# Kernel tuning notes

Hardware: AMD Instinct MI355X
Metric: run time of the kernel (lower is better)

Reference implementation:

```python
import jax, jax.numpy as jnp
import numpy as np

# ---- static config (seq_lens / is_prefill are Python lists in the original) ----
HIDDEN, H, D = 4096, 32, 128
SEQ = 1024            # prefill length / decode history length
N_PRE, N_DEC = 4, 4
T = N_PRE * SEQ + N_DEC            # 4100 total tokens
SEQ_LENS = [SEQ] * N_PRE + [SEQ] * N_DEC
IS_PREFILL = [True] * N_PRE + [False] * N_DEC
NUM_SLOTS = 8192
MAX_LEN, ROPE_BASE = 8192, 10000.0
SCALE = D ** -0.5


def _rope_tables():
    inv_freq = 1.0 / (ROPE_BASE ** (np.arange(0, D, 2, dtype=np.float32) / D))
    t = np.arange(MAX_LEN, dtype=np.float32)
    freqs = np.outer(t, inv_freq)
    emb = np.concatenate([freqs, freqs], axis=-1)  # [MAX_LEN, D]
    return jnp.asarray(np.cos(emb), jnp.float32), jnp.asarray(np.sin(emb), jnp.float32)

COS_T, SIN_T = _rope_tables()


def rotate_half(x):
    x1, x2 = jnp.split(x, 2, axis=-1)
    return jnp.concatenate([-x2, x1], axis=-1)


def setup_inputs() -> dict:
    key = jax.random.key(0)
    k1, k2, k3 = jax.random.split(key, 3)
    x = jax.random.normal(k1, (T, HIDDEN), jnp.float32)
    # positions: prefill seqs get 0..SEQ-1, decode seqs are at position SEQ
    pos = np.concatenate([np.tile(np.arange(SEQ), N_PRE), np.full(N_DEC, SEQ)]).astype(np.int64)
    positions = jnp.asarray(pos)
    slot_mapping = jnp.arange(T, dtype=jnp.int64)
    k_cache = jnp.zeros((NUM_SLOTS, H, D), jnp.float32)
    v_cache = jnp.zeros((NUM_SLOTS, H, D), jnp.float32)
    w_qkv = jax.random.normal(k2, (HIDDEN, 3 * H * D), jnp.float32) * 0.02
    w_out = jax.random.normal(k3, (H * D, HIDDEN), jnp.float32) * 0.02
    return {"x": x, "k_cache": k_cache, "v_cache": v_cache, "w_qkv": w_qkv,
            "w_out": w_out, "positions": positions, "slot_mapping": slot_mapping}


def reference(x, k_cache, v_cache, w_qkv, w_out, positions, slot_mapping):
    qkv = x @ w_qkv                                   # [T, 3*H*D]
    q, k, v = jnp.split(qkv, 3, axis=-1)
    q = q.reshape(T, H, D)
    k = k.reshape(T, H, D)
    v = v.reshape(T, H, D)
    cos = COS_T[positions][:, None, :]                # [T, 1, D]
    sin = SIN_T[positions][:, None, :]
    q = q * cos + rotate_half(q) * sin
    k = k * cos + rotate_half(k) * sin
    # scatter new k/v into flat paged cache
    kc = k_cache.at[slot_mapping].set(k)
    vc = v_cache.at[slot_mapping].set(v)

    outs = []
    off = 0
    for seq_len, prefill in zip(SEQ_LENS, IS_PREFILL):
        nq = seq_len if prefill else 1
        q_i = q[off:off + nq]                         # [nq, H, D]
        if prefill:
            k_i, v_i = k[off:off + nq], v[off:off + nq]
            attn = jnp.einsum('qhd,khd->hqk', q_i, k_i) * SCALE
            mask = jnp.triu(jnp.full((nq, nq), -jnp.inf, jnp.float32), 1)
            attn = jax.nn.softmax(attn + mask, axis=-1)
            out = jnp.einsum('hqk,khd->qhd', attn, v_i).reshape(nq, H * D)
        else:
            k_h, v_h = kc[:seq_len], vc[:seq_len]     # history from cache
            attn = jnp.einsum('qhd,khd->hqk', q_i, k_h) * SCALE
            attn = jax.nn.softmax(attn, axis=-1)
            out = jnp.einsum('hqk,khd->qhd', attn, v_h).reshape(1, H * D)
        outs.append(out)
        off += nq
    return jnp.concatenate(outs, axis=0) @ w_out      # [T, HIDDEN]
```

## Files before the change

kernel.cpp:

```cpp
#include <hip/hip_runtime.h>

#define T_TOK 4100
#define MMAIN 4096
#define HID   4096
#define NH    32
#define DH    128
#define NQKV  12288
#define ATT_SCALE 0.08838834764831845f
#define NEG_BIG  (-3.0e38f)

typedef unsigned short ushort_t;
typedef __attribute__((ext_vector_type(8))) short bf16x8;
typedef __attribute__((ext_vector_type(4))) float f32x4;

typedef const void __attribute__((address_space(1)))* gas_ptr;
typedef void __attribute__((address_space(3)))* las_ptr;

__device__ __forceinline__ ushort_t f2bf(float f){
  unsigned int u = __builtin_bit_cast(unsigned int, f);
  u = u + 0x7FFFu + ((u >> 16) & 1u);
  return (ushort_t)(u >> 16);
}
__device__ __forceinline__ float bf2f(ushort_t h){
  unsigned int u = ((unsigned int)h) << 16;
  return __builtin_bit_cast(float, u);
}
__device__ __forceinline__ f32x4 mfma16(bf16x8 a, bf16x8 b, f32x4 c){
  return __builtin_amdgcn_mfma_f32_16x16x32_bf16(a, b, c, 0, 0, 0);
}
__device__ __forceinline__ void gload_lds16(const void* g, void* l){
  __builtin_amdgcn_global_load_lds((gas_ptr)g, (las_ptr)l, 16, 0, 0);
}


__global__ void convert_x(const float* __restrict__ x, ushort_t* __restrict__ xb){
  const long i4 = (long)blockIdx.x * 256 + threadIdx.x;
  if (i4 >= (long)T_TOK * HID / 4) return;
  const long i = i4 * 4;
  const float4 v = *(const float4*)(x + i);
  union { ushort_t u[4]; uint2 w; } o;
  o.u[0] = f2bf(v.x); o.u[1] = f2bf(v.y); o.u[2] = f2bf(v.z); o.u[3] = f2bf(v.w);
  *(uint2*)(xb + i) = o.w;
}

__global__ void tconv(const float* __restrict__ W, ushort_t* __restrict__ WT, int R, int C){
  __shared__ float tile[32][33];
  const int bc = blockIdx.x, br = blockIdx.y;
  const int tid = threadIdx.x;
  const int cl = tid & 31, rl = tid >> 5;
  const long c = (long)bc * 32 + cl;
#pragma unroll
  for (int j = 0; j < 32; j += 8)
    tile[rl + j][cl] = W[((long)br * 32 + rl + j) * C + c];
  __syncthreads();
#pragma unroll
  for (int j = 0; j < 32; j += 8)
    WT[((long)bc * 32 + rl + j) * R + (long)br * 32 + cl] = f2bf(tile[cl][rl + j]);
}


#define MFMAQ(QM,QN,BARR)                                                         \
  _Pragma("unroll")                                                               \
  for (int mi = 0; mi < 4; ++mi) {                                                \
    _Pragma("unroll")                                                             \
    for (int ni = 0; ni < 2; ++ni) {                                              \
      acc[QM][QN][mi][ni] = mfma16(af[mi][0], BARR[ni][0], acc[QM][QN][mi][ni]);  \
      acc[QM][QN][mi][ni] = mfma16(af[mi][1], BARR[ni][1], acc[QM][QN][mi][ni]);  \
    } }

template<bool OUT_BF16>
__global__ void __launch_bounds__(512, 2)
gemm256(const ushort_t* __restrict__ A, const ushort_t* __restrict__ B,
        ushort_t* __restrict__ Cb, float* __restrict__ Cf,
        int N, int K, int GM, int Mvalid)
{
  extern __shared__ char smem[];
  char* smA = smem;
  char* smB = smem + 65536;

  const int nwg = gridDim.x;
  int bid = blockIdx.x;
  bid = (bid & 7) * (nwg >> 3) + (bid >> 3);
  const int bm = bid % GM, bn = bid / GM;

  const int tid = threadIdx.x;
  const int wid = tid >> 6, lane = tid & 63;
  const int wm = wid >> 2, wn = wid & 3;
  const int l16 = lane & 15, g = lane >> 4;
  const int lr = lane >> 3, lu = lane & 7;

  const long arow0 = (long)bm * 256;
  const long brow0 = (long)bn * 256;

  const ushort_t* aS[4]; const ushort_t* bS[4];
#pragma unroll
  for (int cc = 0; cc < 4; ++cc){
    aS[cc] = A + (arow0 + cc*64 + wid*8 + lr) * (long)K + (lu ^ lr) * 8;
    bS[cc] = B + (brow0 + cc*64 + wid*8 + lr) * (long)K + (lu ^ lr) * 8;
  }

  auto stageA = [&](int buf, int cc, long kt){
    gload_lds16(aS[cc] + kt, smA + buf*32768 + (cc*64 + wid*8)*128);
  };
  auto stageB = [&](int buf, int cc, long kt){
    gload_lds16(bS[cc] + kt, smB + buf*32768 + (cc*64 + wid*8)*128);
  };
  auto ldA = [&](int buf, int qm, int mi, int ks) -> bf16x8 {
    const int row = qm*128 + wm*64 + mi*16 + l16;
    return *(const bf16x8*)(smA + buf*32768 + row*128 + (((ks*4+g) ^ (l16&7))*16));
  };
  auto ldB = [&](int buf, int qn, int ni, int ks) -> bf16x8 {
    const int row = qn*128 + wn*32 + ni*16 + l16;
    return *(const bf16x8*)(smB + buf*32768 + row*128 + (((ks*4+g) ^ (l16&7))*16));
  };

  f32x4 acc[2][2][4][2];
#pragma unroll
  for (int a_ = 0; a_ < 2; ++a_)
#pragma unroll
  for (int b_ = 0; b_ < 2; ++b_)
#pragma unroll
  for (int c_ = 0; c_ < 4; ++c_)
#pragma unroll
  for (int d_ = 0; d_ < 2; ++d_) acc[a_][b_][c_][d_] = (f32x4){0.f,0.f,0.f,0.f};

  bf16x8 af[4][2], bf0[2][2], bf1[2][2];
  const int NT = K >> 6;

  stageA(0,0,0); stageA(0,1,0);
  stageB(0,0,0); stageB(0,1,0);
  stageB(0,2,0); stageB(0,3,0);
  stageA(0,2,0); stageA(0,3,0);
  asm volatile("s_waitcnt vmcnt(4)" ::: "memory");
  __builtin_amdgcn_s_barrier();

  auto tile = [&](int buf, long ktn){
    asm volatile("s_waitcnt vmcnt(2)" ::: "memory");
#pragma unroll
    for (int mi = 0; mi < 4; ++mi){ af[mi][0] = ldA(buf,0,mi,0); af[mi][1] = ldA(buf,0,mi,1); }
#pragma unroll
    for (int ni = 0; ni < 2; ++ni){ bf0[ni][0] = ldB(buf,0,ni,0); bf0[ni][1] = ldB(buf,0,ni,1); }
    stageA(buf^1, 0, ktn); stageA(buf^1, 1, ktn);
    __builtin_amdgcn_s_barrier();
    asm volatile("s_waitcnt lgkmcnt(0)" ::: "memory");
    __builtin_amdgcn_sched_barrier(0);
    __builtin_amdgcn_s_setprio(1);
    MFMAQ(0,0,bf0);
    __builtin_amdgcn_s_setprio(0);
    asm volatile("s_waitcnt vmcnt(2)" ::: "memory");
#pragma unroll
    for (int ni = 0; ni < 2; ++ni){ bf1[ni][0] = ldB(buf,1,ni,0); bf1[ni][1] = ldB(buf,1,ni,1); }
    stageB(buf^1, 0, ktn); stageB(buf^1, 1, ktn);
    __builtin_amdgcn_s_barrier();
    asm volatile("s_waitcnt lgkmcnt(0)" ::: "memory");
    __builtin_amdgcn_sched_barrier(0);
    __builtin_amdgcn_s_setprio(1);
    MFMAQ(0,1,bf1);
    __builtin_amdgcn_s_setprio(0);
#pragma unroll
    for (int mi = 0; mi < 4; ++mi){ af[mi][0] = ldA(buf,1,mi,0); af[mi][1] = ldA(buf,1,mi,1); }
    stageB(buf^1, 2, ktn); stageB(buf^1, 3, ktn);
    __builtin_amdgcn_s_barrier();
    asm volatile("s_waitcnt lgkmcnt(0)" ::: "memory");
    __builtin_amdgcn_sched_barrier(0);
    __builtin_amdgcn_s_setprio(1);
    MFMAQ(1,1,bf1);
    __builtin_amdgcn_s_setprio(0);
    asm volatile("s_waitcnt vmcnt(2)" ::: "memory");
    stageA(buf^1, 2, ktn); stageA(buf^1, 3, ktn);
    __builtin_amdgcn_s_barrier();
    __builtin_amdgcn_sched_barrier(0);
    __builtin_amdgcn_s_setprio(1);
    MFMAQ(1,0,bf0);
    __builtin_amdgcn_s_setprio(0);
  };

  for (int t = 0; t < NT; t += 2){
    const long k1 = (long)(t+1) * 64;
    const long k2 = (long)((t+2 < NT) ? (t+2) : (NT-1)) * 64;
    tile(0, k1);
    tile(1, k2);
  }
  asm volatile("s_waitcnt vmcnt(0)" ::: "memory");

#pragma unroll
  for (int qm = 0; qm < 2; ++qm)
#pragma unroll
  for (int qn = 0; qn < 2; ++qn)
#pragma unroll
  for (int mi = 0; mi < 4; ++mi)
#pragma unroll
  for (int ni = 0; ni < 2; ++ni)
#pragma unroll
  for (int r = 0; r < 4; ++r){
    const long row = arow0 + qm*128 + wm*64 + mi*16 + g*4 + r;
    const long col = brow0 + qn*128 + wn*32 + ni*16 + l16;
    if (OUT_BF16){
      Cb[row * N + col] = f2bf(acc[qm][qn][mi][ni][r]);
    } else {
      if (row < Mvalid) Cf[row * N + col] = acc[qm][qn][mi][ni][r];
    }
  }
}


__global__ void __launch_bounds__(256, 8)
gemv_tail(const ushort_t* __restrict__ A, const ushort_t* __restrict__ B,
          ushort_t* __restrict__ Cb, float* __restrict__ Cf, int ldc)
{
  const int col  = blockIdx.x * 4 + (threadIdx.x >> 6);
  const int lane = threadIdx.x & 63;
  const ushort_t* brow  = B + (long)col * HID + lane * 64;
  const ushort_t* abase = A + 4096L * HID + lane * 64;
  float acc0 = 0.f, acc1 = 0.f, acc2 = 0.f, acc3 = 0.f;
#pragma unroll
  for (int i = 0; i < 8; ++i){
    union { bf16x8 v; short s[8]; } bv, a0, a1, a2, a3;
    bv.v = *(const bf16x8*)(brow + i*8);
    a0.v = *(const bf16x8*)(abase + 0L*HID + i*8);
    a1.v = *(const bf16x8*)(abase + 1L*HID + i*8);
    a2.v = *(const bf16x8*)(abase + 2L*HID + i*8);
    a3.v = *(const bf16x8*)(abase + 3L*HID + i*8);
#pragma unroll
    for (int e = 0; e < 8; ++e){
      const float bf_ = bf2f((ushort_t)bv.s[e]);
      acc0 += bf2f((ushort_t)a0.s[e]) * bf_;
      acc1 += bf2f((ushort_t)a1.s[e]) * bf_;
      acc2 += bf2f((ushort_t)a2.s[e]) * bf_;
      acc3 += bf2f((ushort_t)a3.s[e]) * bf_;
    }
  }
#pragma unroll
  for (int off = 32; off; off >>= 1){
    acc0 += __shfl_xor(acc0, off);
    acc1 += __shfl_xor(acc1, off);
    acc2 += __shfl_xor(acc2, off);
    acc3 += __shfl_xor(acc3, off);
  }
  if (lane == 0){
    if (Cb){
      Cb[4096L*ldc + col] = f2bf(acc0);
      Cb[4097L*ldc + col] = f2bf(acc1);
      Cb[4098L*ldc + col] = f2bf(acc2);
      Cb[4099L*ldc + col] = f2bf(acc3);
    } else {
      Cf[4096L*ldc + col] = acc0;
      Cf[4097L*ldc + col] = acc1;
      Cf[4098L*ldc + col] = acc2;
      Cf[4099L*ldc + col] = acc3;
    }
  }
}


__global__ void rope_scatter(ushort_t* __restrict__ qkv,
                             const int* __restrict__ pos32,
                             const int* __restrict__ slot32,
                             ushort_t* __restrict__ kcw, ushort_t* __restrict__ vcw)
{
  const long gi = (long)blockIdx.x * 256 + threadIdx.x;
  if (gi >= (long)T_TOK * NH * 64) return;
  const int  i = gi & 63;
  const int  h = (gi >> 6) & 31;
  const long t = gi >> 11;

  const bool p64 = (pos32[1] == 0);
  const bool s64 = (slot32[1] == 0);
  const long pv   = p64 ? ((const long long*)pos32)[t]  : (long)pos32[t];
  const long slot = s64 ? ((const long long*)slot32)[t] : (long)slot32[t];

  const float inv = exp2f(-(float)i * 0.2076187116f);
  const float ang = (float)pv * inv;
  float sn, cs;
  __sincosf(ang, &sn, &cs);

  ushort_t* base = qkv + t * (long)NQKV + h * DH + i;
  const float q1 = bf2f(base[0]), q2 = bf2f(base[64]);
  base[0]  = f2bf(q1 * cs - q2 * sn);
  base[64] = f2bf(q2 * cs + q1 * sn);

  if (t < 4096){
    ushort_t* kb = base + HID;
    const float k1 = bf2f(kb[0]), k2 = bf2f(kb[64]);
    const float k1n = k1 * cs - k2 * sn, k2n = k2 * cs + k1 * sn;
    kb[0]  = f2bf(k1n);
    kb[64] = f2bf(k2n);

    if (slot >= 0 && slot < 1024){
      ushort_t* kd = kcw + (slot * NH + h) * DH + i;
      kd[0] = f2bf(k1n); kd[64] = f2bf(k2n);
      const ushort_t* vsrc = base + 2 * HID;
      ushort_t* vd = vcw + (slot * NH + h) * DH + i;
      vd[0] = vsrc[0]; vd[64] = vsrc[64];
    }
  }
}


__global__ void __launch_bounds__(256, 3)
attn_fused(const ushort_t* __restrict__ qkv, const ushort_t* __restrict__ kcw,
           const ushort_t* __restrict__ vcw, ushort_t* __restrict__ attn)
{
  __shared__ char sm[44032];
  const int B = blockIdx.x;
  const int xcd = B & 7, s = B >> 3;
  const int gw = s / 17, q = s % 17;
  const int g_ = gw * 8 + xcd;
  const int h = g_ >> 2, sq = g_ & 3;
  const int qb = (q == 16) ? 16 : 15 - q;
  const int tid = threadIdx.x, wid = tid >> 6, lane = tid & 63;

  if (qb == 16){
    float* qs  = (float*)sm;
    float* ps  = qs + 128;
    float* red = ps + 1024;
    float* oh  = red + 8;
    const long t = 4096 + sq;
    if (tid < 128) qs[tid] = bf2f(qkv[t * (long)NQKV + h*DH + tid]);
    __syncthreads();
    float sv[4];
#pragma unroll
    for (int j = 0; j < 4; j++){
      const int key = tid + j*256;
      const ushort_t* kr = kcw + ((long)key * NH + h) * DH;
      float acc = 0.f;
      for (int d = 0; d < 128; d += 8){
        union { bf16x8 v; short s8[8]; } uu;
        uu.v = *(const bf16x8*)(kr + d);
#pragma unroll
        for (int e = 0; e < 8; e++) acc += qs[d+e] * bf2f((ushort_t)uu.s8[e]);
      }
      sv[j] = acc * ATT_SCALE;
    }
    float mx = fmaxf(fmaxf(sv[0], sv[1]), fmaxf(sv[2], sv[3]));
#pragma unroll
    for (int off = 1; off < 64; off <<= 1) mx = fmaxf(mx, __shfl_xor(mx, off));
    if (lane == 0) red[wid] = mx;
    __syncthreads();
    const float gmax = fmaxf(fmaxf(red[0], red[1]), fmaxf(red[2], red[3]));
    float psum = 0.f;
#pragma unroll
    for (int j = 0; j < 4; j++){
      const float p = __expf(sv[j] - gmax);
      ps[tid + j*256] = p;
      psum += p;
    }
#pragma unroll
    for (int off = 1; off < 64; off <<= 1) psum += __shfl_xor(psum, off);
    if (lane == 0) red[4 + wid] = psum;
    __syncthreads();
    const float gsum = red[4] + red[5] + red[6] + red[7];
    const int d = tid & 127, half = tid >> 7;
    float acc = 0.f;
    for (int key = half*512; key < half*512 + 512; ++key)
      acc += ps[key] * bf2f(vcw[((long)key * NH + h) * DH + d]);
    if (half) oh[d] = acc;
    __syncthreads();
    if (!half) attn[t * HID + h*DH + d] = f2bf((acc + oh[d]) / gsum);
    return;
  }

  ushort_t (*Ks)[128]    = (ushort_t(*)[128])sm;
  ushort_t (*Vt)[72]     = (ushort_t(*)[72])(sm + 16384);
  ushort_t (*Ps)[16][72] = (ushort_t(*)[16][72])(sm + 34816);
  const long tok0 = (long)sq * 1024;
  const int l16 = lane & 15, g = lane >> 4;
  const int q0 = qb * 64;

  bf16x8 qf[4];
  {
    const ushort_t* qrow = qkv + (tok0 + q0 + wid*16 + l16) * (long)NQKV + h * DH;
#pragma unroll
    for (int dc = 0; dc < 4; ++dc) qf[dc] = *(const bf16x8*)(qrow + dc*32 + g*8);
  }

  bf16x8 vones;
  {
    union { ushort_t u[8]; bf16x8 v; } one_;
#pragma unroll
    for (int e = 0; e < 8; ++e) one_.u[e] = 0x3F80;
    vones = one_.v;
  }

  f32x4 oacc[8];
#pragma unroll
  for (int i = 0; i < 8; i++) oacc[i] = (f32x4){0.f, 0.f, 0.f, 0.f};
  f32x4 lacc = (f32x4){0.f, 0.f, 0.f, 0.f};

  const int nkb = qb + 1;
  for (int kb = 0; kb < nkb; ++kb){
    __syncthreads();
    {
      const ushort_t* kbase = qkv + (tok0 + kb*64) * (long)NQKV + HID + h * DH;
#pragma unroll
      for (int c = 0; c < 4; ++c){
        const int row = c*16 + wid*4 + g;
        const int pu = (l16 & 8) | ((l16 ^ (row & 7)) & 7);
        gload_lds16(kbase + (long)row * NQKV + pu*8, &Ks[c*16 + wid*4][0]);
      }
    }
    {
      const int key4 = (tid & 15) * 4;
      const int dg8  = tid >> 4;
      const ushort_t* vbase = qkv + (tok0 + kb*64) * (long)NQKV + 2*HID + h*DH + dg8*8;
      union { bf16x8 v; short s8[8]; } vr[4];
#pragma unroll
      for (int j = 0; j < 4; ++j)
        vr[j].v = *(const bf16x8*)(vbase + (long)(key4 + j) * NQKV);
#pragma unroll
      for (int e = 0; e < 8; ++e){
        union { ushort_t u[4]; uint2 w; } o;
        o.u[0] = (ushort_t)vr[0].s8[e]; o.u[1] = (ushort_t)vr[1].s8[e];
        o.u[2] = (ushort_t)vr[2].s8[e]; o.u[3] = (ushort_t)vr[3].s8[e];
        *(uint2*)&Vt[dg8*8 + e][key4] = o.w;
      }
    }
    __syncthreads();

    {
      f32x4 sfr[4];
#pragma unroll
      for (int nf = 0; nf < 4; ++nf) sfr[nf] = (f32x4){0.f,0.f,0.f,0.f};
      __builtin_amdgcn_s_setprio(1);
#pragma unroll
      for (int nf = 0; nf < 4; ++nf){
#pragma unroll
        for (int dc = 0; dc < 4; ++dc){
          const int uu = dc*4 + g;
          const int pu = (uu & 8) | ((uu ^ (l16 & 7)) & 7);
          bf16x8 kf = *(const bf16x8*)&Ks[nf*16 + l16][pu * 8];
          sfr[nf] = mfma16(qf[dc], kf, sfr[nf]);
        }
      }
      __builtin_amdgcn_s_setprio(0);
      const bool diag = (kb == qb);
#pragma unroll
      for (int r = 0; r < 4; r++){
        float s4[4];
#pragma unroll
        for (int nf = 0; nf < 4; ++nf) s4[nf] = sfr[nf][r] * ATT_SCALE;
        if (diag){
          const int qg = q0 + wid*16 + g*4 + r;
#pragma unroll
          for (int nf = 0; nf < 4; ++nf)
            if (kb*64 + nf*16 + l16 > qg) s4[nf] = NEG_BIG;
        }
#pragma unroll
        for (int nf = 0; nf < 4; ++nf)
          Ps[wid][g*4 + r][nf*16 + l16] = f2bf(__expf(s4[nf]));
      }
      __builtin_amdgcn_s_setprio(1);
#pragma unroll
      for (int ks = 0; ks < 2; ++ks){
        bf16x8 pa = *(const bf16x8*)&Ps[wid][l16][ks*32 + g*8];
        lacc = mfma16(pa, vones, lacc);
#pragma unroll
        for (int df = 0; df < 8; ++df){
          bf16x8 vf = *(const bf16x8*)&Vt[df*16 + l16][ks*32 + g*8];
          oacc[df] = mfma16(pa, vf, oacc[df]);
        }
      }
      __builtin_amdgcn_s_setprio(0);
    }
  }

#pragma unroll
  for (int df = 0; df < 8; ++df){
#pragma unroll
    for (int r = 0; r < 4; ++r){
      const long row = tok0 + q0 + wid*16 + g*4 + r;
      attn[row * HID + h*DH + df*16 + l16] = f2bf(oacc[df][r] / lacc[r]);
    }
  }
}


extern "C" void kernel_launch(void* const* d_in, const int* in_sizes, int n_in,
                              void* d_out, int out_size, void* d_ws, size_t ws_size,
                              hipStream_t stream) {
  const float* x      = (const float*)d_in[0];
  const float* wqkv   = (const float*)d_in[3];
  const float* wout   = (const float*)d_in[4];
  const int*   pos    = (const int*)d_in[5];
  const int*   slots  = (const int*)d_in[6];

  char* ws = (char*)d_ws;
  ushort_t* xb    = (ushort_t*)(ws);
  ushort_t* qkvb  = (ushort_t*)(ws + 35651584L);
  ushort_t* wqkvT = (ushort_t*)(ws + 142606336L);
  ushort_t* attnb = (ushort_t*)(ws + 142606336L);
  ushort_t* woutT = (ushort_t*)(ws + 243269632L);
  ushort_t* kcw   = (ushort_t*)(ws + 276824064L);
  ushort_t* vcw   = (ushort_t*)(ws + 285212672L);

  hipFuncSetAttribute((const void*)gemm256<true>,
                      hipFuncAttributeMaxDynamicSharedMemorySize, 131072);
  hipFuncSetAttribute((const void*)gemm256<false>,
                      hipFuncAttributeMaxDynamicSharedMemorySize, 131072);

  convert_x<<<16400, 256, 0, stream>>>(x, xb);
  tconv<<<dim3(NQKV/32, HID/32), 256, 0, stream>>>(wqkv, wqkvT, HID, NQKV);
  tconv<<<dim3(HID/32, HID/32), 256, 0, stream>>>(wout, woutT, HID, HID);

  gemm256<true><<<(MMAIN/256)*(NQKV/256), 512, 131072, stream>>>(
      xb, wqkvT, qkvb, nullptr, NQKV, HID, MMAIN/256, MMAIN);
  gemv_tail<<<HID/4, 256, 0, stream>>>(xb, wqkvT, qkvb, nullptr, NQKV);

  rope_scatter<<<32800, 256, 0, stream>>>(qkvb, pos, slots, kcw, vcw);

  attn_fused<<<2176, 256, 0, stream>>>(qkvb, kcw, vcw, attnb);

  gemm256<false><<<(MMAIN/256)*(HID/256), 512, 131072, stream>>>(
      attnb, woutT, nullptr, (float*)d_out, HID, HID, MMAIN/256, MMAIN);
  gemv_tail<<<HID/4, 256, 0, stream>>>(attnb, woutT, nullptr, (float*)d_out, HID);

  (void)in_sizes; (void)n_in; (void)out_size; (void)ws_size;
}
```

Before: 862.9 us.

## Vectorize conversion, transpose, and RoPE kernels; simplify attention grid mapping

convert_x becomes a grid-stride loop over a fixed grid of 2048 blocks. tconv moves to 64x64 tiles with float4 loads and 16-byte bf16 stores, and rope_scatter now handles 8 elements per thread with 128-bit loads and stores. The attention kernel drops its XCD-aware swizzled block index for a plain 3D grid with query blocks in ascending order, which may hurt L2 locality and the big-blocks-first load balancing. These changes aim to cut memory-transaction overhead in the preprocessing kernels.

```diff
diff --git a/kernel.cpp b/kernel.cpp
--- a/kernel.cpp
+++ b/kernel.cpp
@@ -34,28 +34,37 @@
 
 
 __global__ void convert_x(const float* __restrict__ x, ushort_t* __restrict__ xb){
-  const long i4 = (long)blockIdx.x * 256 + threadIdx.x;
-  if (i4 >= (long)T_TOK * HID / 4) return;
-  const long i = i4 * 4;
-  const float4 v = *(const float4*)(x + i);
-  union { ushort_t u[4]; uint2 w; } o;
-  o.u[0] = f2bf(v.x); o.u[1] = f2bf(v.y); o.u[2] = f2bf(v.z); o.u[3] = f2bf(v.w);
-  *(uint2*)(xb + i) = o.w;
+  const long nvec = (long)T_TOK * HID / 4;
+  for (long i4 = (long)blockIdx.x * 256 + threadIdx.x; i4 < nvec; i4 += 2048L * 256){
+    const long i = i4 * 4;
+    const float4 v = *(const float4*)(x + i);
+    union { ushort_t u[4]; uint2 w; } o;
+    o.u[0] = f2bf(v.x); o.u[1] = f2bf(v.y); o.u[2] = f2bf(v.z); o.u[3] = f2bf(v.w);
+    *(uint2*)(xb + i) = o.w;
+  }
 }
 
 __global__ void tconv(const float* __restrict__ W, ushort_t* __restrict__ WT, int R, int C){
-  __shared__ float tile[32][33];
+  __shared__ float tile[64][65];
   const int bc = blockIdx.x, br = blockIdx.y;
   const int tid = threadIdx.x;
-  const int cl = tid & 31, rl = tid >> 5;
-  const long c = (long)bc * 32 + cl;
-#pragma unroll
-  for (int j = 0; j < 32; j += 8)
-    tile[rl + j][cl] = W[((long)br * 32 + rl + j) * C + c];
+  const int c4 = tid & 15, r0 = tid >> 4;
+  const long cbase = (long)bc * 64 + c4 * 4;
+#pragma unroll
+  for (int j = 0; j < 4; ++j){
+    const int r = r0 + j*16;
+    const float4 v = *(const float4*)(W + ((long)br*64 + r) * C + cbase);
+    tile[r][c4*4+0] = v.x; tile[r][c4*4+1] = v.y;
+    tile[r][c4*4+2] = v.z; tile[r][c4*4+3] = v.w;
+  }
   __syncthreads();
-#pragma unroll
-  for (int j = 0; j < 32; j += 8)
-    WT[((long)bc * 32 + rl + j) * R + (long)br * 32 + cl] = f2bf(tile[cl][rl + j]);
+  const int c = tid >> 2, rseg = (tid & 3) * 16;
+  union { ushort_t u[16]; uint4 w[2]; } o;
+#pragma unroll
+  for (int e = 0; e < 16; ++e) o.u[e] = f2bf(tile[rseg + e][c]);
+  ushort_t* dst = WT + ((long)bc*64 + c) * R + (long)br*64 + rseg;
+  *(uint4*)(dst)     = o.w[0];
+  *(uint4*)(dst + 8) = o.w[1];
 }
 
 
@@ -259,39 +268,61 @@
                              ushort_t* __restrict__ kcw, ushort_t* __restrict__ vcw)
 {
   const long gi = (long)blockIdx.x * 256 + threadIdx.x;
-  if (gi >= (long)T_TOK * NH * 64) return;
-  const int  i = gi & 63;
-  const int  h = (gi >> 6) & 31;
-  const long t = gi >> 11;
+  if (gi >= (long)T_TOK * NH * 8) return;
+  const int  i8 = gi & 7;
+  const int  h  = (gi >> 3) & 31;
+  const long t  = gi >> 8;
 
   const bool p64 = (pos32[1] == 0);
   const bool s64 = (slot32[1] == 0);
   const long pv   = p64 ? ((const long long*)pos32)[t]  : (long)pos32[t];
   const long slot = s64 ? ((const long long*)slot32)[t] : (long)slot32[t];
 
-  const float inv = exp2f(-(float)i * 0.2076187116f);
-  const float ang = (float)pv * inv;
-  float sn, cs;
-  __sincosf(ang, &sn, &cs);
-
-  ushort_t* base = qkv + t * (long)NQKV + h * DH + i;
-  const float q1 = bf2f(base[0]), q2 = bf2f(base[64]);
-  base[0]  = f2bf(q1 * cs - q2 * sn);
-  base[64] = f2bf(q2 * cs + q1 * sn);
+  float cs[8], sn[8];
+#pragma unroll
+  for (int e = 0; e < 8; ++e){
+    const int i = i8*8 + e;
+    const float inv = exp2f(-(float)i * 0.2076187116f);
+    __sincosf((float)pv * inv, &sn[e], &cs[e]);
+  }
+
+  ushort_t* base = qkv + t * (long)NQKV + h * DH + i8*8;
+  {
+    union { bf16x8 v; short s[8]; } lo, hi;
+    lo.v = *(const bf16x8*)(base);
+    hi.v = *(const bf16x8*)(base + 64);
+#pragma unroll
+    for (int e = 0; e < 8; ++e){
+      const float a = bf2f((ushort_t)lo.s[e]), b = bf2f((ushort_t)hi.s[e]);
+      lo.s[e] = (short)f2bf(a * cs[e] - b * sn[e]);
+      hi.s[e] = (short)f2bf(b * cs[e] + a * sn[e]);
+    }
+    *(bf16x8*)(base)      = lo.v;
+    *(bf16x8*)(base + 64) = hi.v;
+  }
 
   if (t < 4096){
     ushort_t* kb = base + HID;
-    const float k1 = bf2f(kb[0]), k2 = bf2f(kb[64]);
-    const float k1n = k1 * cs - k2 * sn, k2n = k2 * cs + k1 * sn;
-    kb[0]  = f2bf(k1n);
-    kb[64] = f2bf(k2n);
+    union { bf16x8 v; short s[8]; } lo, hi;
+    lo.v = *(const bf16x8*)(kb);
+    hi.v = *(const bf16x8*)(kb + 64);
+#pragma unroll
+    for (int e = 0; e < 8; ++e){
+      const float a = bf2f((ushort_t)lo.s[e]), b = bf2f((ushort_t)hi.s[e]);
+      lo.s[e] = (short)f2bf(a * cs[e] - b * sn[e]);
+      hi.s[e] = (short)f2bf(b * cs[e] + a * sn[e]);
+    }
+    *(bf16x8*)(kb)      = lo.v;
+    *(bf16x8*)(kb + 64) = hi.v;
 
     if (slot >= 0 && slot < 1024){
-      ushort_t* kd = kcw + (slot * NH + h) * DH + i;
-      kd[0] = f2bf(k1n); kd[64] = f2bf(k2n);
+      ushort_t* kd = kcw + (slot * NH + h) * DH + i8*8;
+      *(bf16x8*)(kd)      = lo.v;
+      *(bf16x8*)(kd + 64) = hi.v;
       const ushort_t* vsrc = base + 2 * HID;
-      ushort_t* vd = vcw + (slot * NH + h) * DH + i;
-      vd[0] = vsrc[0]; vd[64] = vsrc[64];
+      ushort_t* vd = vcw + (slot * NH + h) * DH + i8*8;
+      *(bf16x8*)(vd)      = *(const bf16x8*)(vsrc);
+      *(bf16x8*)(vd + 64) = *(const bf16x8*)(vsrc + 64);
     }
   }
 }
@@ -302,12 +333,7 @@
            const ushort_t* __restrict__ vcw, ushort_t* __restrict__ attn)
 {
   __shared__ char sm[44032];
-  const int B = blockIdx.x;
-  const int xcd = B & 7, s = B >> 3;
-  const int gw = s / 17, q = s % 17;
-  const int g_ = gw * 8 + xcd;
-  const int h = g_ >> 2, sq = g_ & 3;
-  const int qb = (q == 16) ? 16 : 15 - q;
+  const int qb = blockIdx.x, h = blockIdx.y, sq = blockIdx.z;
   const int tid = threadIdx.x, wid = tid >> 6, lane = tid & 63;
 
   if (qb == 16){
@@ -498,17 +524,17 @@
   hipFuncSetAttribute((const void*)gemm256<false>,
                       hipFuncAttributeMaxDynamicSharedMemorySize, 131072);
 
-  convert_x<<<16400, 256, 0, stream>>>(x, xb);
-  tconv<<<dim3(NQKV/32, HID/32), 256, 0, stream>>>(wqkv, wqkvT, HID, NQKV);
-  tconv<<<dim3(HID/32, HID/32), 256, 0, stream>>>(wout, woutT, HID, HID);
+  convert_x<<<2048, 256, 0, stream>>>(x, xb);
+  tconv<<<dim3(NQKV/64, HID/64), 256, 0, stream>>>(wqkv, wqkvT, HID, NQKV);
+  tconv<<<dim3(HID/64, HID/64), 256, 0, stream>>>(wout, woutT, HID, HID);
 
   gemm256<true><<<(MMAIN/256)*(NQKV/256), 512, 131072, stream>>>(
       xb, wqkvT, qkvb, nullptr, NQKV, HID, MMAIN/256, MMAIN);
   gemv_tail<<<HID/4, 256, 0, stream>>>(xb, wqkvT, qkvb, nullptr, NQKV);
 
-  rope_scatter<<<32800, 256, 0, stream>>>(qkvb, pos, slots, kcw, vcw);
-
-  attn_fused<<<2176, 256, 0, stream>>>(qkvb, kcw, vcw, attnb);
+  rope_scatter<<<4100, 256, 0, stream>>>(qkvb, pos, slots, kcw, vcw);
+
+  attn_fused<<<dim3(17, NH, 4), 256, 0, stream>>>(qkvb, kcw, vcw, attnb);
 
   gemm256<false><<<(MMAIN/256)*(HID/256), 512, 131072, stream>>>(
       attnb, woutT, nullptr, (float*)d_out, HID, HID, MMAIN/256, MMAIN);
```

New measurement: 812.5 us, median of 2. 5.8% less time.
